# Kernel tuning notes

Hardware: AMD Instinct MI355X
Metric: run time of the kernel (lower is better)

## Reference

```python
import jax, jax.numpy as jnp
import numpy as np

N = 100000      # nodes
E = 1600000     # edges (avg degree 16)
DIN = 128       # input feature dim
DOUT = 64       # per-head output dim
H = 4           # independent heads, mean-aggregated
LRELU_ALPHA = 0.2  # tf.nn.leaky_relu default


def setup_inputs() -> dict:
    key = jax.random.key(0)
    k = jax.random.split(key, 7)
    inputs = jax.random.normal(k[0], (N, DIN), dtype=jnp.float32)
    edge_row = jnp.sort(jax.random.randint(k[1], (E,), 0, N, dtype=jnp.int32))
    edge_col = jax.random.randint(k[2], (E,), 0, N, dtype=jnp.int32)
    edge_val = jnp.ones((E,), dtype=jnp.float32)  # binary adjacency values
    # Glorot-ish scaled params per head
    W = jax.random.normal(k[3], (H, DIN, DOUT), dtype=jnp.float32) * np.float32(1.0 / np.sqrt(DIN))
    a1 = jax.random.normal(k[4], (H, DOUT), dtype=jnp.float32) * np.float32(1.0 / np.sqrt(DOUT))
    a2 = jax.random.normal(k[5], (H, DOUT), dtype=jnp.float32) * np.float32(1.0 / np.sqrt(DOUT))
    b = jnp.zeros((H, DOUT), dtype=jnp.float32)  # contrib.layers.bias_add bias
    return {"inputs": inputs, "W": W, "a1": a1, "a2": a2, "b": b,
            "edge_val": edge_val, "edge_row": edge_row, "edge_col": edge_col}


def _gat_head(inputs, Wh, a1h, a2h, bh, edge_val, edge_row, edge_col):
    xh = inputs @ Wh                          # [N, DOUT]  per-head projection
    f1 = jax.nn.elu(xh @ a1h)                 # [N]  Dense(D,1, act=elu) on key=x
    f2 = jax.nn.elu(xh @ a2h)                 # [N]
    # sparse_add of adj*f1 (row-broadcast) and adj*f2^T (col-broadcast)
    le = jax.nn.leaky_relu(edge_val * (f1[edge_row] + f2[edge_col]), LRELU_ALPHA)  # [E]
    # sparse softmax per destination row (reverse_axis=1)
    m = jax.ops.segment_max(le, edge_row, num_segments=N)        # [N]
    ex = jnp.exp(le - m[edge_row])                               # [E]
    s = jax.ops.segment_sum(ex, edge_row, num_segments=N)        # [N]
    coef = ex / s[edge_row]                                      # [E]
    # sparse_dense_matmul: out[r] = sum_e coef_e * x[col_e]
    out = jax.ops.segment_sum(coef[:, None] * xh[edge_col], edge_row, num_segments=N)  # [N, DOUT]
    return jax.nn.elu(out + bh)


def reference(inputs, W, a1, a2, b, edge_val, edge_row, edge_col):
    res = jnp.zeros((N, DOUT), dtype=inputs.dtype)
    for h in range(H):  # small fixed head count; each head has independent weights
        res = res + _gat_head(inputs, W[h], a1[h], a2[h], b[h], edge_val, edge_row, edge_col)
    return res / H
```

## Files before the change

kernel.cpp:

```cpp
#include <hip/hip_runtime.h>

#define NN 100000
#define EE 1600000
#define DIN 128
#define DOUT 64
#define NH 4

typedef __attribute__((ext_vector_type(8))) short bf16x8;
typedef __attribute__((ext_vector_type(4))) float f32x4;

__device__ __forceinline__ float elu_f(float x) {
  return x > 0.f ? x : (__expf(x) - 1.f);
}
__device__ __forceinline__ float lrelu_f(float x) {
  return x > 0.f ? x : 0.2f * x;
}
__device__ __forceinline__ float b2f(unsigned short u) {
  union { unsigned int i; float f; } v; v.i = ((unsigned int)u) << 16; return v.f;
}
__device__ __forceinline__ unsigned short f2b(float f) {
  union { float f; unsigned int i; } v; v.f = f;
  unsigned int r = v.i + 0x7fffu + ((v.i >> 16) & 1u);
  return (unsigned short)(r >> 16);
}

__global__ __launch_bounds__(256) void wbf_k(
    const float* __restrict__ W, unsigned short* __restrict__ wbt) {
  int idx = blockIdx.x * 256 + threadIdx.x;
  int col = idx >> 7, k = idx & 127;
  int h = col >> 6, j = col & 63;
  wbt[idx] = f2b(W[(size_t)h * DIN * DOUT + k * DOUT + j]);
}

__global__ __launch_bounds__(256) void build_row_ptr_k(
    const int* __restrict__ erow, int* __restrict__ rp) {
  int r = blockIdx.x * 256 + threadIdx.x;
  if (r > NN) return;
  int lo = 0, hi = EE;
  while (lo < hi) {
    int mid = (lo + hi) >> 1;
    if (erow[mid] < r) lo = mid + 1; else hi = mid;
  }
  rp[r] = lo;
}

__global__ __launch_bounds__(256) void proj_mfma_k(
    const float* __restrict__ inp, const unsigned short* __restrict__ wbt,
    const float* __restrict__ a1, const float* __restrict__ a2,
    float* __restrict__ f1p, float* __restrict__ f2p,
    unsigned short* __restrict__ xh) {
  __shared__ unsigned short lds_a[64 * 128];
  const int tid = threadIdx.x;
  const int h = tid >> 6;
  const int l = tid & 63;
  const int lr = l & 15;
  const int lk = l >> 4;
  const int row0 = blockIdx.x * 64;

  #pragma unroll
  for (int i = 0; i < 8; ++i) {
    const int idx = i * 256 + tid;
    const int row = idx >> 5;
    const int c4 = idx & 31;
    int grow = row0 + row;
    if (grow >= NN) grow = NN - 1;
    const float4 v = *(const float4*)(inp + (size_t)grow * DIN + c4 * 4);
    ushort4 w;
    w.x = f2b(v.x); w.y = f2b(v.y); w.z = f2b(v.z); w.w = f2b(v.w);
    const int byte_off = row * 256 + ((c4 * 8) ^ ((row & 7) << 4));
    *(ushort4*)((char*)lds_a + byte_off) = w;
  }

  bf16x8 bf[4][4];
  #pragma unroll
  for (int n = 0; n < 4; ++n) {
    const int col = h * DOUT + n * 16 + lr;
    #pragma unroll
    for (int kc = 0; kc < 4; ++kc)
      bf[n][kc] = *(const bf16x8*)(wbt + (size_t)col * DIN + kc * 32 + lk * 8);
  }
  __syncthreads();

  f32x4 acc[4][4];
  #pragma unroll
  for (int m = 0; m < 4; ++m)
    #pragma unroll
    for (int n = 0; n < 4; ++n)
      acc[m][n] = (f32x4)(0.f);

  #pragma unroll
  for (int m = 0; m < 4; ++m) {
    const int r = m * 16 + lr;
    bf16x8 af[4];
    #pragma unroll
    for (int kc = 0; kc < 4; ++kc)
      af[kc] = *(const bf16x8*)((char*)lds_a + r * 256 +
                                ((kc * 64 + lk * 16) ^ ((r & 7) << 4)));
    #pragma unroll
    for (int kc = 0; kc < 4; ++kc)
      #pragma unroll
      for (int n = 0; n < 4; ++n)
        acc[m][n] = __builtin_amdgcn_mfma_f32_16x16x32_bf16(
            bf[n][kc], af[kc], acc[m][n], 0, 0, 0);
  }

  float4 a1q[4], a2q[4];
  #pragma unroll
  for (int n = 0; n < 4; ++n) {
    a1q[n] = *(const float4*)(a1 + h * DOUT + n * 16 + lk * 4);
    a2q[n] = *(const float4*)(a2 + h * DOUT + n * 16 + lk * 4);
  }
  #pragma unroll
  for (int m = 0; m < 4; ++m) {
    const int row = row0 + m * 16 + lr;
    const bool ok = row < NN;
    float p1 = 0.f, p2 = 0.f;
    #pragma unroll
    for (int n = 0; n < 4; ++n) {
      const f32x4 a = acc[m][n];
      ushort4 pk;
      pk.x = f2b(a[0]); pk.y = f2b(a[1]); pk.z = f2b(a[2]); pk.w = f2b(a[3]);
      if (ok)
        *(ushort4*)(xh + (size_t)row * (NH * DOUT) + h * DOUT + n * 16 + lk * 4) = pk;
      p1 = fmaf(a[0], a1q[n].x, p1); p1 = fmaf(a[1], a1q[n].y, p1);
      p1 = fmaf(a[2], a1q[n].z, p1); p1 = fmaf(a[3], a1q[n].w, p1);
      p2 = fmaf(a[0], a2q[n].x, p2); p2 = fmaf(a[1], a2q[n].y, p2);
      p2 = fmaf(a[2], a2q[n].z, p2); p2 = fmaf(a[3], a2q[n].w, p2);
    }
    p1 += __shfl_xor(p1, 16); p1 += __shfl_xor(p1, 32);
    p2 += __shfl_xor(p2, 16); p2 += __shfl_xor(p2, 32);
    if (ok && lk == 0) {
      f1p[(size_t)row * NH + h] = elu_f(p1);
      f2p[(size_t)row * NH + h] = elu_f(p2);
    }
  }
}

__global__ __launch_bounds__(256) void agg_k(
    const int* __restrict__ rp, const int* __restrict__ ecol,
    const float* __restrict__ eval, const float* __restrict__ f1p,
    const float* __restrict__ f2p, const unsigned short* __restrict__ xh,
    const float* __restrict__ b, float* __restrict__ out) {
  const int tid = threadIdx.x;
  const int wave = tid >> 6, lane = tid & 63;
  const int r = blockIdx.x * 4 + wave;
  if (r >= NN) return;
  const int g = lane >> 4;
  int e0 = __builtin_amdgcn_readfirstlane(rp[r]);
  int e1 = __builtin_amdgcn_readfirstlane(rp[r + 1]);
  const float f1r = f1p[(size_t)r * NH + g];
  float ax = 0.f, ay = 0.f, az = 0.f, aw = 0.f;
  float ssum = 0.f;
  int e = e0;
  for (; e + 8 <= e1; e += 8) {
    int c[8]; float vv[8];
    #pragma unroll
    for (int u = 0; u < 8; ++u) { c[u] = ecol[e + u]; vv[u] = eval[e + u]; }
    ushort4 xv[8]; float f2v[8];
    #pragma unroll
    for (int u = 0; u < 8; ++u) {
      xv[u] = *(const ushort4*)(xh + (size_t)c[u] * (NH * DOUT) + lane * 4);
      f2v[u] = f2p[(size_t)c[u] * NH + g];
    }
    #pragma unroll
    for (int u = 0; u < 8; ++u) {
      const float ex = __expf(lrelu_f(vv[u] * (f1r + f2v[u])));
      ssum += ex;
      ax = fmaf(ex, b2f(xv[u].x), ax);
      ay = fmaf(ex, b2f(xv[u].y), ay);
      az = fmaf(ex, b2f(xv[u].z), az);
      aw = fmaf(ex, b2f(xv[u].w), aw);
    }
  }
  if (e < e1) {
    int c[8]; float vv[8]; bool okk[8];
    #pragma unroll
    for (int u = 0; u < 8; ++u) {
      int ee = e + u;
      okk[u] = ee < e1;
      if (!okk[u]) ee = e1 - 1;
      c[u] = ecol[ee]; vv[u] = eval[ee];
    }
    ushort4 xv[8]; float f2v[8];
    #pragma unroll
    for (int u = 0; u < 8; ++u) {
      xv[u] = *(const ushort4*)(xh + (size_t)c[u] * (NH * DOUT) + lane * 4);
      f2v[u] = f2p[(size_t)c[u] * NH + g];
    }
    #pragma unroll
    for (int u = 0; u < 8; ++u) {
      float ex = __expf(lrelu_f(vv[u] * (f1r + f2v[u])));
      ex = okk[u] ? ex : 0.f;
      ssum += ex;
      ax = fmaf(ex, b2f(xv[u].x), ax);
      ay = fmaf(ex, b2f(xv[u].y), ay);
      az = fmaf(ex, b2f(xv[u].z), az);
      aw = fmaf(ex, b2f(xv[u].w), aw);
    }
  }
  const float4 bb = *(const float4*)(b + lane * 4);
  const float inv = (e1 > e0) ? (1.f / ssum) : 0.f;
  float v0 = elu_f(ax * inv + bb.x);
  float v1 = elu_f(ay * inv + bb.y);
  float v2 = elu_f(az * inv + bb.z);
  float v3 = elu_f(aw * inv + bb.w);
  v0 += __shfl_xor(v0, 16); v1 += __shfl_xor(v1, 16);
  v2 += __shfl_xor(v2, 16); v3 += __shfl_xor(v3, 16);
  v0 += __shfl_xor(v0, 32); v1 += __shfl_xor(v1, 32);
  v2 += __shfl_xor(v2, 32); v3 += __shfl_xor(v3, 32);
  if (lane < 16) {
    f32x4 o = {v0 * 0.25f, v1 * 0.25f, v2 * 0.25f, v3 * 0.25f};
    __builtin_nontemporal_store(o, (f32x4*)(out + (size_t)r * DOUT + lane * 4));
  }
}

extern "C" void kernel_launch(void* const* d_in, const int* in_sizes, int n_in,
                              void* d_out, int out_size, void* d_ws, size_t ws_size,
                              hipStream_t stream) {
  const float* inp = (const float*)d_in[0];
  const float* W   = (const float*)d_in[1];
  const float* a1  = (const float*)d_in[2];
  const float* a2  = (const float*)d_in[3];
  const float* b   = (const float*)d_in[4];
  const float* ev  = (const float*)d_in[5];
  const int* erow  = (const int*)d_in[6];
  const int* ecol  = (const int*)d_in[7];
  float* out = (float*)d_out;

  char* ws = (char*)d_ws;
  size_t off = 0;
  int* rp = (int*)(ws + off);
  off += (((size_t)(NN + 1) * 4) + 255) & ~(size_t)255;
  float* f1p = (float*)(ws + off);
  off += (((size_t)NH * NN * 4) + 255) & ~(size_t)255;
  float* f2p = (float*)(ws + off);
  off += (((size_t)NH * NN * 4) + 255) & ~(size_t)255;
  unsigned short* xh = (unsigned short*)(ws + off);
  off += (((size_t)NN * NH * DOUT * 2) + 255) & ~(size_t)255;
  unsigned short* wbt = (unsigned short*)(ws + off);

  wbf_k<<<(NH * DIN * DOUT) / 256, 256, 0, stream>>>(W, wbt);
  build_row_ptr_k<<<(NN + 1 + 255) / 256, 256, 0, stream>>>(erow, rp);
  proj_mfma_k<<<(NN + 63) / 64, 256, 0, stream>>>(inp, wbt, a1, a2, f1p, f2p, xh);
  agg_k<<<(NN + 3) / 4, 256, 0, stream>>>(rp, ecol, ev, f1p, f2p, xh, b, out);
}
```

Before: 177.2 us.

## Split each wave into two half-waves processing alternate edges with 16-byte gathers

The aggregation kernel now splits each wave into two 32-lane halves. Each half handles alternate edges of the row, and each lane gathers 8 bf16 values (16 bytes) instead of 4. This doubles the number of edges in flight per iteration and widens the gather loads. The cost is more accumulator registers and an extra cross-half reduction before normalisation. Leaky ReLU is also rewritten as fmaxf.

Result: no change. 180.2 us (+1.7%).

```diff
diff --git a/kernel.cpp b/kernel.cpp
--- a/kernel.cpp
+++ b/kernel.cpp
@@ -7,13 +7,11 @@
 #define NH 4
 
 typedef __attribute__((ext_vector_type(8))) short bf16x8;
+typedef __attribute__((ext_vector_type(8))) unsigned short u16x8;
 typedef __attribute__((ext_vector_type(4))) float f32x4;
 
 __device__ __forceinline__ float elu_f(float x) {
   return x > 0.f ? x : (__expf(x) - 1.f);
-}
-__device__ __forceinline__ float lrelu_f(float x) {
-  return x > 0.f ? x : 0.2f * x;
 }
 __device__ __forceinline__ float b2f(unsigned short u) {
   union { unsigned int i; float f; } v; v.i = ((unsigned int)u) << 16; return v.f;
@@ -145,72 +143,84 @@
   const int wave = tid >> 6, lane = tid & 63;
   const int r = blockIdx.x * 4 + wave;
   if (r >= NN) return;
-  const int g = lane >> 4;
-  int e0 = __builtin_amdgcn_readfirstlane(rp[r]);
-  int e1 = __builtin_amdgcn_readfirstlane(rp[r + 1]);
+  const int half = lane >> 5;
+  const int local = lane & 31;
+  const int g = local >> 3;
+  int rb = __builtin_amdgcn_readfirstlane(rp[r]);
+  int re = __builtin_amdgcn_readfirstlane(rp[r + 1]);
   const float f1r = f1p[(size_t)r * NH + g];
-  float ax = 0.f, ay = 0.f, az = 0.f, aw = 0.f;
+  float acc[8];
+  #pragma unroll
+  for (int j = 0; j < 8; ++j) acc[j] = 0.f;
   float ssum = 0.f;
-  int e = e0;
-  for (; e + 8 <= e1; e += 8) {
-    int c[8]; float vv[8];
-    #pragma unroll
-    for (int u = 0; u < 8; ++u) { c[u] = ecol[e + u]; vv[u] = eval[e + u]; }
-    ushort4 xv[8]; float f2v[8];
-    #pragma unroll
-    for (int u = 0; u < 8; ++u) {
-      xv[u] = *(const ushort4*)(xh + (size_t)c[u] * (NH * DOUT) + lane * 4);
-      f2v[u] = f2p[(size_t)c[u] * NH + g];
-    }
-    #pragma unroll
-    for (int u = 0; u < 8; ++u) {
-      const float ex = __expf(lrelu_f(vv[u] * (f1r + f2v[u])));
+  int e = rb;
+  for (; e + 16 <= re; e += 16) {
+    int cc[8]; float vv[8];
+    #pragma unroll
+    for (int p = 0; p < 8; ++p) {
+      const int ee = e + 2 * p + half;
+      cc[p] = ecol[ee]; vv[p] = eval[ee];
+    }
+    u16x8 xv[8]; float f2v[8];
+    #pragma unroll
+    for (int p = 0; p < 8; ++p) {
+      xv[p] = *(const u16x8*)(xh + (size_t)cc[p] * (NH * DOUT) + local * 8);
+      f2v[p] = f2p[(size_t)cc[p] * NH + g];
+    }
+    #pragma unroll
+    for (int p = 0; p < 8; ++p) {
+      const float t = vv[p] * (f1r + f2v[p]);
+      const float ex = __expf(fmaxf(t, 0.2f * t));
       ssum += ex;
-      ax = fmaf(ex, b2f(xv[u].x), ax);
-      ay = fmaf(ex, b2f(xv[u].y), ay);
-      az = fmaf(ex, b2f(xv[u].z), az);
-      aw = fmaf(ex, b2f(xv[u].w), aw);
-    }
-  }
-  if (e < e1) {
-    int c[8]; float vv[8]; bool okk[8];
-    #pragma unroll
-    for (int u = 0; u < 8; ++u) {
-      int ee = e + u;
-      okk[u] = ee < e1;
-      if (!okk[u]) ee = e1 - 1;
-      c[u] = ecol[ee]; vv[u] = eval[ee];
-    }
-    ushort4 xv[8]; float f2v[8];
-    #pragma unroll
-    for (int u = 0; u < 8; ++u) {
-      xv[u] = *(const ushort4*)(xh + (size_t)c[u] * (NH * DOUT) + lane * 4);
-      f2v[u] = f2p[(size_t)c[u] * NH + g];
-    }
-    #pragma unroll
-    for (int u = 0; u < 8; ++u) {
-      float ex = __expf(lrelu_f(vv[u] * (f1r + f2v[u])));
-      ex = okk[u] ? ex : 0.f;
+      #pragma unroll
+      for (int j = 0; j < 8; ++j)
+        acc[j] = fmaf(ex, b2f((unsigned short)xv[p][j]), acc[j]);
+    }
+  }
+  if (e < re) {
+    int cc[8]; float vv[8]; bool ok[8];
+    #pragma unroll
+    for (int p = 0; p < 8; ++p) {
+      int ee = e + 2 * p + half;
+      ok[p] = ee < re;
+      if (!ok[p]) ee = re - 1;
+      cc[p] = ecol[ee]; vv[p] = eval[ee];
+    }
+    u16x8 xv[8]; float f2v[8];
+    #pragma unroll
+    for (int p = 0; p < 8; ++p) {
+      xv[p] = *(const u16x8*)(xh + (size_t)cc[p] * (NH * DOUT) + local * 8);
+      f2v[p] = f2p[(size_t)cc[p] * NH + g];
+    }
+    #pragma unroll
+    for (int p = 0; p < 8; ++p) {
+      const float t = vv[p] * (f1r + f2v[p]);
+      float ex = __expf(fmaxf(t, 0.2f * t));
+      ex = ok[p] ? ex : 0.f;
       ssum += ex;
-      ax = fmaf(ex, b2f(xv[u].x), ax);
-      ay = fmaf(ex, b2f(xv[u].y), ay);
-      az = fmaf(ex, b2f(xv[u].z), az);
-      aw = fmaf(ex, b2f(xv[u].w), aw);
-    }
-  }
-  const float4 bb = *(const float4*)(b + lane * 4);
-  const float inv = (e1 > e0) ? (1.f / ssum) : 0.f;
-  float v0 = elu_f(ax * inv + bb.x);
-  float v1 = elu_f(ay * inv + bb.y);
-  float v2 = elu_f(az * inv + bb.z);
-  float v3 = elu_f(aw * inv + bb.w);
-  v0 += __shfl_xor(v0, 16); v1 += __shfl_xor(v1, 16);
-  v2 += __shfl_xor(v2, 16); v3 += __shfl_xor(v3, 16);
-  v0 += __shfl_xor(v0, 32); v1 += __shfl_xor(v1, 32);
-  v2 += __shfl_xor(v2, 32); v3 += __shfl_xor(v3, 32);
-  if (lane < 16) {
-    f32x4 o = {v0 * 0.25f, v1 * 0.25f, v2 * 0.25f, v3 * 0.25f};
-    __builtin_nontemporal_store(o, (f32x4*)(out + (size_t)r * DOUT + lane * 4));
+      #pragma unroll
+      for (int j = 0; j < 8; ++j)
+        acc[j] = fmaf(ex, b2f((unsigned short)xv[p][j]), acc[j]);
+    }
+  }
+  ssum += __shfl_xor(ssum, 32);
+  #pragma unroll
+  for (int j = 0; j < 8; ++j) acc[j] += __shfl_xor(acc[j], 32);
+  const float inv = (re > rb) ? (1.f / ssum) : 0.f;
+  float o[8];
+  #pragma unroll
+  for (int j = 0; j < 8; ++j) {
+    o[j] = elu_f(acc[j] * inv + b[local * 8 + j]);
+    o[j] += __shfl_xor(o[j], 8);
+    o[j] += __shfl_xor(o[j], 16);
+    o[j] *= 0.25f;
+  }
+  if (lane < 8) {
+    f32x4 o0 = {o[0], o[1], o[2], o[3]};
+    f32x4 o1 = {o[4], o[5], o[6], o[7]};
+    f32x4* dst = (f32x4*)(out + (size_t)r * DOUT + local * 8);
+    __builtin_nontemporal_store(o0, dst);
+    __builtin_nontemporal_store(o1, dst + 1);
   }
 }
 
```
